# Performance work log

Hardware: AMD Instinct MI355X
Metric: run time of the kernel (lower is better)

The kernel has to match this reference:

```python
import jax, jax.numpy as jnp
import numpy as np

DIM = 1024
HID = 2048
E = 4

def setup_inputs() -> dict:
    key = jax.random.key(0)
    ks = jax.random.split(key, 7)
    s = lambda fan_in: 1.0 / np.sqrt(fan_in)
    x = jax.random.normal(ks[0], (2, 2048, DIM), dtype=jnp.float32)
    W1 = jax.random.uniform(ks[1], (E, DIM, HID), jnp.float32, -s(DIM), s(DIM))
    b1 = jax.random.uniform(ks[2], (E, HID), jnp.float32, -s(DIM), s(DIM))
    W2 = jax.random.uniform(ks[3], (E, HID, DIM), jnp.float32, -s(HID), s(HID))
    b2 = jax.random.uniform(ks[4], (E, DIM), jnp.float32, -s(HID), s(HID))
    Wr = jax.random.uniform(ks[5], (DIM, E), jnp.float32, -s(DIM), s(DIM))
    br = jax.random.uniform(ks[6], (E,), jnp.float32, -s(DIM), s(DIM))
    return {"x": x, "W1": W1, "b1": b1, "W2": W2, "b2": b2, "Wr": Wr, "br": br}

def reference(x, W1, b1, W2, b2, Wr, br):
    # router softmax weights: [B,T,E]
    weights = jax.nn.softmax(x @ Wr + br, axis=-1)
    # all-expert MLP: hidden [B,T,E,H]
    h = jax.nn.gelu(jnp.einsum('btd,edh->bteh', x, W1) + b1, approximate=False)
    # expert outputs [B,T,E,D]
    y = jnp.einsum('bteh,ehd->bted', h, W2) + b2
    # softmax-weighted combine over experts
    return jnp.einsum('bte,bted->btd', weights, y)
```

## Files before the change

kernel.cpp:

```cpp
#include <hip/hip_runtime.h>
#include <hip/hip_bf16.h>
#include <math.h>

#define DIM 1024
#define HID 2048
#define NE  4
#define NT  4096
#define KW  (NE*HID)
#define KSPLIT 4
#define KCH (KW / KSPLIT)

typedef __attribute__((ext_vector_type(8))) short short8;
typedef __attribute__((ext_vector_type(4))) short short4v;
typedef __attribute__((ext_vector_type(4))) float floatx4;


__device__ __forceinline__ void async_cp16(const void* g, void* l) {
  __builtin_amdgcn_global_load_lds(
      (const __attribute__((address_space(1))) void*)g,
      (__attribute__((address_space(3))) void*)l, 16, 0, 0);
}

__device__ __forceinline__ short f2bf(float f) {
  union { float f; unsigned u; } x; x.f = f;
  unsigned r = x.u + 0x7fffu + ((x.u >> 16) & 1u);
  return (short)(r >> 16);
}

__device__ __forceinline__ float gelu_fast(float v) {
  float u = 1.595769122f * (v + 0.044715f * v * v * v);
  return v * __builtin_amdgcn_rcpf(1.0f + __expf(-u));
}

__global__ void router_kernel(const float* __restrict__ x,
                              const float* __restrict__ Wr,
                              const float* __restrict__ br,
                              float* __restrict__ wgt) {
  const int wv = threadIdx.x >> 6, lane = threadIdx.x & 63;
  const int t = blockIdx.x * 4 + wv;
  const float* xr = x + (size_t)t * DIM;
  float a0 = 0.f, a1 = 0.f, a2 = 0.f, a3 = 0.f;
  for (int d = lane; d < DIM; d += 64) {
    float xv = xr[d];
    floatx4 wr = *(const floatx4*)&Wr[d * 4];
    a0 += xv * wr[0]; a1 += xv * wr[1]; a2 += xv * wr[2]; a3 += xv * wr[3];
  }
  #pragma unroll
  for (int off = 32; off; off >>= 1) {
    a0 += __shfl_down(a0, off);
    a1 += __shfl_down(a1, off);
    a2 += __shfl_down(a2, off);
    a3 += __shfl_down(a3, off);
  }
  a0 = __shfl(a0, 0); a1 = __shfl(a1, 0); a2 = __shfl(a2, 0); a3 = __shfl(a3, 0);
  float s0 = a0 + br[0], s1 = a1 + br[1], s2 = a2 + br[2], s3 = a3 + br[3];
  float m = fmaxf(fmaxf(s0, s1), fmaxf(s2, s3));
  float e0 = __expf(s0 - m), e1 = __expf(s1 - m), e2 = __expf(s2 - m), e3 = __expf(s3 - m);
  float inv = 1.f / (e0 + e1 + e2 + e3);
  float v = (lane == 0) ? e0 : (lane == 1) ? e1 : (lane == 2) ? e2 : e3;
  if (lane < 4) wgt[t * 4 + lane] = v * inv;
}

__global__ void cvt_x(const float* __restrict__ x, short* __restrict__ xb) {
  int i = (blockIdx.x * 256 + threadIdx.x) * 4;
  floatx4 v = *(const floatx4*)&x[i];
  short4v o;
  o[0] = f2bf(v[0]); o[1] = f2bf(v[1]); o[2] = f2bf(v[2]); o[3] = f2bf(v[3]);
  *(short4v*)&xb[i] = o;
}

__global__ void transpose_cvt(const float* __restrict__ in, short* __restrict__ out,
                              int R, int C) {
  __shared__ float tile[32][33];
  const size_t zo = (size_t)blockIdx.z * R * C;
  in += zo; out += zo;
  const int tx = threadIdx.x, ty = threadIdx.y;
  const int c = blockIdx.x * 32 + tx;
  #pragma unroll
  for (int i = 0; i < 4; i++) {
    int r = blockIdx.y * 32 + ty + i * 8;
    tile[ty + i * 8][tx] = in[(size_t)r * C + c];
  }
  __syncthreads();
  const int r2 = blockIdx.y * 32 + tx;
  #pragma unroll
  for (int i = 0; i < 4; i++) {
    int c2 = blockIdx.x * 32 + ty + i * 8;
    out[(size_t)c2 * R + r2] = f2bf(tile[tx][ty + i * 8]);
  }
}


__global__ __launch_bounds__(256, 2)
void gemm1_kernel(const short* __restrict__ xb, const short* __restrict__ w1t,
                  const float* __restrict__ b1, const float* __restrict__ wgt,
                  short* __restrict__ hw) {
  const int e  = blockIdx.z;
  const int m0 = blockIdx.y * 128;
  const int n0 = blockIdx.x * 128;
  const int tid = threadIdx.x;
  const int lane = tid & 63;
  const int wv = tid >> 6;
  const int wm = (wv >> 1) * 64, wn = (wv & 1) * 64;
  const int quad = lane >> 4, lrow = lane & 15;
  const int sr  = tid >> 3;
  const int kof = ((tid & 7) ^ (sr & 7)) * 8;
  const int rkey = lrow & 7;

  __shared__ __align__(16) short As[128 * 64];
  __shared__ __align__(16) short Bs[128 * 64];

  const short* Ap = xb;
  const short* Bp = w1t + (size_t)e * HID * DIM;

  floatx4 acc[4][4];
  #pragma unroll
  for (int i = 0; i < 4; i++)
    #pragma unroll
    for (int j = 0; j < 4; j++) acc[i][j] = (floatx4)0.f;

  for (int k0 = 0; k0 < DIM; k0 += 64) {
    __syncthreads();
    #pragma unroll
    for (int c = 0; c < 4; c++)
      async_cp16(Ap + (size_t)(m0 + c * 32 + sr) * DIM + k0 + kof,
                 As + (c * 256 + tid) * 8);
    #pragma unroll
    for (int c = 0; c < 4; c++)
      async_cp16(Bp + (size_t)(n0 + c * 32 + sr) * DIM + k0 + kof,
                 Bs + (c * 256 + tid) * 8);
    __syncthreads();
    #pragma unroll
    for (int kk = 0; kk < 2; kk++) {
      short8 af[4], bf[4];
      const int ko = ((kk * 4 + quad) ^ rkey) * 8;
      #pragma unroll
      for (int i = 0; i < 4; i++)
        af[i] = *(const short8*)&As[(wm + i * 16 + lrow) * 64 + ko];
      #pragma unroll
      for (int j = 0; j < 4; j++)
        bf[j] = *(const short8*)&Bs[(wn + j * 16 + lrow) * 64 + ko];
      #pragma unroll
      for (int i = 0; i < 4; i++)
        #pragma unroll
        for (int j = 0; j < 4; j++)
          acc[i][j] = __builtin_amdgcn_mfma_f32_16x16x32_bf16(af[i], bf[j], acc[i][j], 0, 0, 0);
    }
  }

  #pragma unroll
  for (int i = 0; i < 4; i++) {
    const int rbase = m0 + wm + i * 16 + quad * 4;
    float wv4[4];
    #pragma unroll
    for (int r = 0; r < 4; r++) wv4[r] = wgt[(rbase + r) * NE + e];
    #pragma unroll
    for (int j = 0; j < 4; j++) {
      const int col = n0 + wn + j * 16 + lrow;
      const float b = b1[e * HID + col];
      #pragma unroll
      for (int r = 0; r < 4; r++) {
        float v = acc[i][j][r] + b;
        hw[(size_t)(rbase + r) * KW + e * HID + col] = f2bf(wv4[r] * gelu_fast(v));
      }
    }
  }
}

__global__ __launch_bounds__(256, 2)
void gemm2_kernel(const short* __restrict__ hw, const short* __restrict__ w2t,
                  const float* __restrict__ b2, const float* __restrict__ wgt,
                  float* __restrict__ out, float* __restrict__ part) {
  const int kz = blockIdx.z;
  const int m0 = blockIdx.y * 128;
  const int n0 = blockIdx.x * 128;
  const int tid = threadIdx.x;
  const int lane = tid & 63;
  const int wv = tid >> 6;
  const int wm = (wv >> 1) * 64, wn = (wv & 1) * 64;
  const int quad = lane >> 4, lrow = lane & 15;
  const int sr  = tid >> 3;
  const int kof = ((tid & 7) ^ (sr & 7)) * 8;
  const int rkey = lrow & 7;

  __shared__ __align__(16) short As[128 * 64];
  __shared__ __align__(16) short Bs[128 * 64];

  floatx4 acc[4][4];
  #pragma unroll
  for (int i = 0; i < 4; i++)
    #pragma unroll
    for (int j = 0; j < 4; j++) acc[i][j] = (floatx4)0.f;

  const int kbeg = kz * KCH;
  for (int kk0 = 0; kk0 < KCH; kk0 += 64) {
    const int k0 = kbeg + kk0;
    __syncthreads();
    #pragma unroll
    for (int c = 0; c < 4; c++)
      async_cp16(hw + (size_t)(m0 + c * 32 + sr) * KW + k0 + kof,
                 As + (c * 256 + tid) * 8);
    #pragma unroll
    for (int c = 0; c < 4; c++)
      async_cp16(w2t + (size_t)(n0 + c * 32 + sr) * KW + k0 + kof,
                 Bs + (c * 256 + tid) * 8);
    __syncthreads();
    #pragma unroll
    for (int kk = 0; kk < 2; kk++) {
      short8 af[4], bf[4];
      const int ko = ((kk * 4 + quad) ^ rkey) * 8;
      #pragma unroll
      for (int i = 0; i < 4; i++)
        af[i] = *(const short8*)&As[(wm + i * 16 + lrow) * 64 + ko];
      #pragma unroll
      for (int j = 0; j < 4; j++)
        bf[j] = *(const short8*)&Bs[(wn + j * 16 + lrow) * 64 + ko];
      #pragma unroll
      for (int i = 0; i < 4; i++)
        #pragma unroll
        for (int j = 0; j < 4; j++)
          acc[i][j] = __builtin_amdgcn_mfma_f32_16x16x32_bf16(af[i], bf[j], acc[i][j], 0, 0, 0);
    }
  }

  if (kz == 0) {
    #pragma unroll
    for (int i = 0; i < 4; i++) {
      const int rbase = m0 + wm + i * 16 + quad * 4;
      floatx4 wr[4];
      #pragma unroll
      for (int r = 0; r < 4; r++) wr[r] = *(const floatx4*)&wgt[(rbase + r) * NE];
      #pragma unroll
      for (int j = 0; j < 4; j++) {
        const int col = n0 + wn + j * 16 + lrow;
        float b2v[4];
        #pragma unroll
        for (int eI = 0; eI < 4; eI++) b2v[eI] = b2[eI * DIM + col];
        #pragma unroll
        for (int r = 0; r < 4; r++) {
          float bias = wr[r][0] * b2v[0] + wr[r][1] * b2v[1] +
                       wr[r][2] * b2v[2] + wr[r][3] * b2v[3];
          out[(size_t)(rbase + r) * DIM + col] = acc[i][j][r] + bias;
        }
      }
    }
  } else {
    float* p = part + (size_t)(kz - 1) * NT * DIM;
    #pragma unroll
    for (int i = 0; i < 4; i++) {
      const int rbase = m0 + wm + i * 16 + quad * 4;
      #pragma unroll
      for (int j = 0; j < 4; j++) {
        const int col = n0 + wn + j * 16 + lrow;
        #pragma unroll
        for (int r = 0; r < 4; r++)
          p[(size_t)(rbase + r) * DIM + col] = acc[i][j][r];
      }
    }
  }
}

__global__ void reduce_out(float* __restrict__ out, const float* __restrict__ part) {
  int i = (blockIdx.x * 256 + threadIdx.x) * 4;
  floatx4 v = *(const floatx4*)&out[i];
  floatx4 a = *(const floatx4*)&part[i];
  floatx4 b = *(const floatx4*)&part[i + NT * DIM];
  floatx4 c = *(const floatx4*)&part[i + 2 * NT * DIM];
  v = v + a + b + c;
  *(floatx4*)&out[i] = v;
}


extern "C" void kernel_launch(void* const* d_in, const int* in_sizes, int n_in,
                              void* d_out, int out_size, void* d_ws, size_t ws_size,
                              hipStream_t stream) {
  const float* x  = (const float*)d_in[0];
  const float* W1 = (const float*)d_in[1];
  const float* b1 = (const float*)d_in[2];
  const float* W2 = (const float*)d_in[3];
  const float* b2 = (const float*)d_in[4];
  const float* Wr = (const float*)d_in[5];
  const float* br = (const float*)d_in[6];
  float* out = (float*)d_out;

  char* ws = (char*)d_ws;
  float* wgt = (float*)(ws);
  short* w2t = (short*)(ws + 65536);
  short* hw  = (short*)(ws + 65536 + 16777216);
  short* xb  = (short*)(ws + 65536 + 16777216 + 67108864);
  short* w1t = (short*)(ws + 65536 + 16777216 + 67108864 + 8388608);
  float* part= (float*)(ws + 65536 + 16777216 + 67108864);

  hipLaunchKernelGGL(router_kernel, dim3(NT / 4), dim3(256), 0, stream, x, Wr, br, wgt);
  hipLaunchKernelGGL(cvt_x, dim3(NT * DIM / 1024), dim3(256), 0, stream, x, xb);
  hipLaunchKernelGGL(transpose_cvt, dim3(HID / 32, DIM / 32, NE), dim3(32, 8), 0, stream,
                     W1, w1t, DIM, HID);
  hipLaunchKernelGGL(transpose_cvt, dim3(DIM / 32, KW / 32, 1), dim3(32, 8), 0, stream,
                     W2, w2t, KW, DIM);
  hipLaunchKernelGGL(gemm1_kernel, dim3(HID / 128, NT / 128, NE), dim3(256), 0, stream,
                     xb, w1t, b1, wgt, hw);
  hipLaunchKernelGGL(gemm2_kernel, dim3(DIM / 128, NT / 128, KSPLIT), dim3(256), 0, stream,
                     hw, w2t, b2, wgt, out, part);
  hipLaunchKernelGGL(reduce_out, dim3(NT * DIM / 1024), dim3(256), 0, stream, out, part);
}
```

Before: 322.5 us.

## Fuse router with x conversion, vectorize transposes, use atomic split-K reduction

Merges the router softmax and the x-to-bf16 conversion into one kernel so x is read once. The weight transpose-convert kernel now uses 16-byte loads and stores with a bf16 LDS tile. The split-K partial buffers and reduce kernel are replaced by a bias_init kernel that writes the weighted b2 bias into the output, after which gemm2 atomically adds its fp32 tile results. Atomics cut the partial-buffer traffic and one launch, but they add contention on the output and make the summation order nondeterministic.

```diff
diff --git a/kernel.cpp b/kernel.cpp
--- a/kernel.cpp
+++ b/kernel.cpp
@@ -32,18 +32,27 @@
   return v * __builtin_amdgcn_rcpf(1.0f + __expf(-u));
 }
 
-__global__ void router_kernel(const float* __restrict__ x,
-                              const float* __restrict__ Wr,
-                              const float* __restrict__ br,
-                              float* __restrict__ wgt) {
+__global__ void router_cvt(const float* __restrict__ x, const float* __restrict__ Wr,
+                           const float* __restrict__ br, float* __restrict__ wgt,
+                           short* __restrict__ xb) {
   const int wv = threadIdx.x >> 6, lane = threadIdx.x & 63;
   const int t = blockIdx.x * 4 + wv;
   const float* xr = x + (size_t)t * DIM;
+  short* xo = xb + (size_t)t * DIM;
   float a0 = 0.f, a1 = 0.f, a2 = 0.f, a3 = 0.f;
-  for (int d = lane; d < DIM; d += 64) {
-    float xv = xr[d];
-    floatx4 wr = *(const floatx4*)&Wr[d * 4];
-    a0 += xv * wr[0]; a1 += xv * wr[1]; a2 += xv * wr[2]; a3 += xv * wr[3];
+  #pragma unroll
+  for (int p = 0; p < 4; p++) {
+    const int d = p * 256 + lane * 4;
+    floatx4 v = *(const floatx4*)&xr[d];
+    short4v o;
+    #pragma unroll
+    for (int j = 0; j < 4; j++) {
+      o[j] = f2bf(v[j]);
+      floatx4 wr = *(const floatx4*)&Wr[(d + j) * 4];
+      a0 += v[j] * wr[0]; a1 += v[j] * wr[1];
+      a2 += v[j] * wr[2]; a3 += v[j] * wr[3];
+    }
+    *(short4v*)&xo[d] = o;
   }
   #pragma unroll
   for (int off = 32; off; off >>= 1) {
@@ -61,33 +70,45 @@
   if (lane < 4) wgt[t * 4 + lane] = v * inv;
 }
 
-__global__ void cvt_x(const float* __restrict__ x, short* __restrict__ xb) {
-  int i = (blockIdx.x * 256 + threadIdx.x) * 4;
-  floatx4 v = *(const floatx4*)&x[i];
-  short4v o;
-  o[0] = f2bf(v[0]); o[1] = f2bf(v[1]); o[2] = f2bf(v[2]); o[3] = f2bf(v[3]);
-  *(short4v*)&xb[i] = o;
-}
-
-__global__ void transpose_cvt(const float* __restrict__ in, short* __restrict__ out,
-                              int R, int C) {
-  __shared__ float tile[32][33];
-  const size_t zo = (size_t)blockIdx.z * R * C;
-  in += zo; out += zo;
-  const int tx = threadIdx.x, ty = threadIdx.y;
-  const int c = blockIdx.x * 32 + tx;
+#define TP_PADR 136
+__global__ void transpose_cvt_fast(const float* __restrict__ in, short* __restrict__ out,
+                                   int R, int C) {
+  __shared__ __align__(16) short tile[32 * TP_PADR];
+  const size_t zo = (size_t)blockIdx.z * (size_t)R * C;
+  const int c0 = blockIdx.x * 32, r0 = blockIdx.y * 128;
+  const int t = threadIdx.x;
+  const int cin = (t & 7) * 4;
+  const int rin = t >> 3;
   #pragma unroll
   for (int i = 0; i < 4; i++) {
-    int r = blockIdx.y * 32 + ty + i * 8;
-    tile[ty + i * 8][tx] = in[(size_t)r * C + c];
+    const int r = rin + i * 32;
+    floatx4 v = *(const floatx4*)&in[zo + (size_t)(r0 + r) * C + c0 + cin];
+    #pragma unroll
+    for (int j = 0; j < 4; j++)
+      tile[(cin + j) * TP_PADR + r] = f2bf(v[j]);
   }
   __syncthreads();
-  const int r2 = blockIdx.y * 32 + tx;
-  #pragma unroll
-  for (int i = 0; i < 4; i++) {
-    int c2 = blockIdx.x * 32 + ty + i * 8;
-    out[(size_t)c2 * R + r2] = f2bf(tile[tx][ty + i * 8]);
-  }
+  const int ct = t >> 3;
+  #pragma unroll
+  for (int i = 0; i < 2; i++) {
+    const int rc = (t & 7) + 8 * i;
+    short8 vv = *(const short8*)&tile[ct * TP_PADR + rc * 8];
+    *(short8*)&out[zo + (size_t)(c0 + ct) * R + r0 + rc * 8] = vv;
+  }
+}
+
+__global__ void bias_init(const float* __restrict__ wgt, const float* __restrict__ b2,
+                          float* __restrict__ out) {
+  const int i = (blockIdx.x * 256 + threadIdx.x) * 4;
+  const int t = i >> 10, d = i & (DIM - 1);
+  floatx4 w = *(const floatx4*)&wgt[t * 4];
+  floatx4 r = (floatx4)0.f;
+  #pragma unroll
+  for (int e = 0; e < 4; e++) {
+    floatx4 bv = *(const floatx4*)&b2[e * DIM + d];
+    r += w[e] * bv;
+  }
+  *(floatx4*)&out[i] = r;
 }
 
 
@@ -169,8 +190,7 @@
 
 __global__ __launch_bounds__(256, 2)
 void gemm2_kernel(const short* __restrict__ hw, const short* __restrict__ w2t,
-                  const float* __restrict__ b2, const float* __restrict__ wgt,
-                  float* __restrict__ out, float* __restrict__ part) {
+                  float* __restrict__ out) {
   const int kz = blockIdx.z;
   const int m0 = blockIdx.y * 128;
   const int n0 = blockIdx.x * 128;
@@ -223,51 +243,17 @@
     }
   }
 
-  if (kz == 0) {
-    #pragma unroll
-    for (int i = 0; i < 4; i++) {
-      const int rbase = m0 + wm + i * 16 + quad * 4;
-      floatx4 wr[4];
-      #pragma unroll
-      for (int r = 0; r < 4; r++) wr[r] = *(const floatx4*)&wgt[(rbase + r) * NE];
-      #pragma unroll
-      for (int j = 0; j < 4; j++) {
-        const int col = n0 + wn + j * 16 + lrow;
-        float b2v[4];
-        #pragma unroll
-        for (int eI = 0; eI < 4; eI++) b2v[eI] = b2[eI * DIM + col];
-        #pragma unroll
-        for (int r = 0; r < 4; r++) {
-          float bias = wr[r][0] * b2v[0] + wr[r][1] * b2v[1] +
-                       wr[r][2] * b2v[2] + wr[r][3] * b2v[3];
-          out[(size_t)(rbase + r) * DIM + col] = acc[i][j][r] + bias;
-        }
-      }
-    }
-  } else {
-    float* p = part + (size_t)(kz - 1) * NT * DIM;
-    #pragma unroll
-    for (int i = 0; i < 4; i++) {
-      const int rbase = m0 + wm + i * 16 + quad * 4;
-      #pragma unroll
-      for (int j = 0; j < 4; j++) {
-        const int col = n0 + wn + j * 16 + lrow;
-        #pragma unroll
-        for (int r = 0; r < 4; r++)
-          p[(size_t)(rbase + r) * DIM + col] = acc[i][j][r];
-      }
-    }
-  }
-}
-
-__global__ void reduce_out(float* __restrict__ out, const float* __restrict__ part) {
-  int i = (blockIdx.x * 256 + threadIdx.x) * 4;
-  floatx4 v = *(const floatx4*)&out[i];
-  floatx4 a = *(const floatx4*)&part[i];
-  floatx4 b = *(const floatx4*)&part[i + NT * DIM];
-  floatx4 c = *(const floatx4*)&part[i + 2 * NT * DIM];
-  v = v + a + b + c;
-  *(floatx4*)&out[i] = v;
+  #pragma unroll
+  for (int i = 0; i < 4; i++) {
+    const int rbase = m0 + wm + i * 16 + quad * 4;
+    #pragma unroll
+    for (int j = 0; j < 4; j++) {
+      const int col = n0 + wn + j * 16 + lrow;
+      #pragma unroll
+      for (int r = 0; r < 4; r++)
+        atomicAdd(&out[(size_t)(rbase + r) * DIM + col], acc[i][j][r]);
+    }
+  }
 }
 
 
@@ -289,17 +275,15 @@
   short* hw  = (short*)(ws + 65536 + 16777216);
   short* xb  = (short*)(ws + 65536 + 16777216 + 67108864);
   short* w1t = (short*)(ws + 65536 + 16777216 + 67108864 + 8388608);
-  float* part= (float*)(ws + 65536 + 16777216 + 67108864);
-
-  hipLaunchKernelGGL(router_kernel, dim3(NT / 4), dim3(256), 0, stream, x, Wr, br, wgt);
-  hipLaunchKernelGGL(cvt_x, dim3(NT * DIM / 1024), dim3(256), 0, stream, x, xb);
-  hipLaunchKernelGGL(transpose_cvt, dim3(HID / 32, DIM / 32, NE), dim3(32, 8), 0, stream,
+
+  hipLaunchKernelGGL(router_cvt, dim3(NT / 4), dim3(256), 0, stream, x, Wr, br, wgt, xb);
+  hipLaunchKernelGGL(transpose_cvt_fast, dim3(HID / 32, DIM / 128, NE), dim3(256), 0, stream,
                      W1, w1t, DIM, HID);
-  hipLaunchKernelGGL(transpose_cvt, dim3(DIM / 32, KW / 32, 1), dim3(32, 8), 0, stream,
+  hipLaunchKernelGGL(transpose_cvt_fast, dim3(DIM / 32, KW / 128, 1), dim3(256), 0, stream,
                      W2, w2t, KW, DIM);
+  hipLaunchKernelGGL(bias_init, dim3(NT * DIM / 1024), dim3(256), 0, stream, wgt, b2, out);
   hipLaunchKernelGGL(gemm1_kernel, dim3(HID / 128, NT / 128, NE), dim3(256), 0, stream,
                      xb, w1t, b1, wgt, hw);
   hipLaunchKernelGGL(gemm2_kernel, dim3(DIM / 128, NT / 128, KSPLIT), dim3(256), 0, stream,
-                     hw, w2t, b2, wgt, out, part);
-  hipLaunchKernelGGL(reduce_out, dim3(NT * DIM / 1024), dim3(256), 0, stream, out, part);
-}
+                     hw, w2t, out);
+}
```

Measured after the change: 329.3 us. 2.1% more time.
